# Performance work log

Measured on AMD Instinct MI355X. Metric: run time of the kernel, lower is better.

Reference implementation:

```python
import jax, jax.numpy as jnp
import numpy as np

N_NODES = 4096
M_NODES = 8192
DIM = 256


def _symnorm(A):
    # D^{-1/2} A D^{-1/2} with eps, via row/col scaling (same math as diag matmuls)
    d = A.sum(axis=1) + 1e-5
    s = d ** -0.5
    return A * s[:, None] * s[None, :]


def _gat(A, X, W, a_src, a_dst, b):
    # Dense-form GATConv (PyG semantics): edges are nonzeros of A plus self loops.
    N = A.shape[0]
    H, F = a_src.shape
    Xp = (X @ W).reshape(N, H, F)                     # [N, H, F]
    src = jnp.einsum('nhf,hf->nh', Xp, a_src)         # score of source node j
    dst = jnp.einsum('nhf,hf->nh', Xp, a_dst)         # score of target node i
    logits = jax.nn.leaky_relu(dst[:, None, :] + src[None, :, :], negative_slope=0.2)  # [i, j, h]
    mask = (A != 0.0) | jnp.eye(N, dtype=bool)        # add_self_loops=True
    logits = jnp.where(mask[:, :, None], logits, -jnp.inf)
    alpha = jax.nn.softmax(logits, axis=1)            # softmax over neighbors j
    out = jnp.einsum('ijh,jhf->ihf', alpha, Xp).reshape(N, H * F) + b
    return out


def setup_inputs() -> dict:
    key = jax.random.key(0)
    ks = jax.random.split(key, 32)

    def p(i, shape, scale=0.05):
        return jax.random.normal(ks[i], shape, dtype=jnp.float32) * scale

    R = jax.random.normal(ks[0], (N_NODES, N_NODES), dtype=jnp.float32)
    A = jax.nn.relu((R + R.T) * 0.5)
    X = jax.random.normal(ks[1], (N_NODES, DIM), dtype=jnp.float32)
    return dict(
        A=A, X=X,
        # down GT0: GATConv(256, 128, heads=4) -> 512
        Wd0=p(2, (256, 512)), asd0=p(3, (4, 128)), add0=p(4, (4, 128)), bd0=p(5, (512,)),
        # down GT1: GATConv(512, 256, heads=4) -> 1024
        Wd1=p(6, (512, 1024)), asd1=p(7, (4, 256)), add1=p(8, (4, 256)), bd1=p(9, (1024,)),
        # pool projections (Linear(in, 1))
        wp0=p(10, (1, 512)), bp0=p(11, (1,)),
        wp1=p(12, (1, 1024)), bp1=p(13, (1,)),
        # bottom GT: GATConv(1024, 512, heads=2) -> 1024
        Wb=p(14, (1024, 1024)), asb=p(15, (2, 512)), adb=p(16, (2, 512)), bb=p(17, (1024,)),
        # up GT (reversed[0]): GATConv(1024, 128, heads=4) -> 512
        Wu0=p(18, (1024, 512)), asu0=p(19, (4, 128)), adu0=p(20, (4, 128)), bu0=p(21, (512,)),
        # up GT (reversed[1]): GATConv(512, 64, heads=4) -> 256
        Wu1=p(22, (512, 256)), asu1=p(23, (4, 64)), adu1=p(24, (4, 64)), bu1=p(25, (256,)),
        # upsampler Linear(n_nodes, m_nodes)
        Wup=p(26, (M_NODES, N_NODES)), bup=p(27, (M_NODES,)),
    )


def reference(A, X, Wd0, asd0, add0, bd0, Wd1, asd1, add1, bd1, wp0, bp0, wp1, bp1,
              Wb, asb, adb, bb, Wu0, asu0, adu0, bu0, Wu1, asu1, adu1, bu1, Wup, bup):
    N0 = A.shape[0]
    A0 = A + jnp.eye(N0, dtype=A.dtype)  # A_ = A + I (used throughout; normalized A is dead code)

    # ---- down level 0 ----
    X0 = jax.nn.relu(_gat(A0, X, Wd0, asd0, add0, bd0))            # [4096, 512]
    s0 = jax.nn.sigmoid(X0 @ wp0[0] + bp0[0])
    k0 = max(2, N0 // 2)                                            # int(0.5 * N)
    v0, idx0 = jax.lax.top_k(s0, k0)
    A1 = _symnorm(A0[idx0][:, idx0])                                # [2048, 2048]
    X1in = X0[idx0] * v0[:, None]

    # ---- down level 1 ----
    X1 = jax.nn.relu(_gat(A1, X1in, Wd1, asd1, add1, bd1))          # [2048, 1024]
    s1 = jax.nn.sigmoid(X1 @ wp1[0] + bp1[0])
    k1 = max(2, k0 // 2)
    v1, idx1 = jax.lax.top_k(s1, k1)
    A2 = _symnorm(A1[idx1][:, idx1])                                # [1024, 1024]
    X2in = X1[idx1] * v1[:, None]

    # ---- bottom ----
    Xb = jax.nn.relu(_gat(A2, X2in, Wb, asb, adb, bb))              # [1024, 1024]

    # ---- up level 0: unpool to level-1 graph ----
    h = jnp.zeros((k0, Xb.shape[1]), Xb.dtype).at[idx1].set(Xb)
    Xu0 = jax.nn.relu(_gat(A1, h, Wu0, asu0, adu0, bu0))            # [2048, 512]
    rec0 = jax.nn.relu(Xu0 @ Xu0.T)

    # ---- up level 1: unpool to original graph ----
    h = jnp.zeros((N0, Xu0.shape[1]), Xu0.dtype).at[idx0].set(Xu0)
    Xu1 = jax.nn.relu(_gat(A0, h, Wu1, asu1, adu1, bu1))            # [4096, 256]
    rec1 = jax.nn.relu(Xu1 @ Xu1.T)

    # ---- upsampler: Linear over node dim, softmax over feature dim, reconstruct adjacency ----
    Z = jax.nn.softmax(Wup @ Xu1 + bup[:, None], axis=1)            # [8192, 256]
    A_up = jax.nn.relu(Z @ Z.T)                                     # [8192, 8192]
    return (A_up, A0, A1, rec0, rec1)
```

## Files before the change

kernel.cpp:

```cpp
#include <hip/hip_runtime.h>
#include <math.h>


typedef short bf16x8 __attribute__((ext_vector_type(8)));
typedef float f32x4 __attribute__((ext_vector_type(4)));

static __device__ __forceinline__ float wave_sum64(float v) {
#pragma unroll
  for (int off = 32; off; off >>= 1) v += __shfl_down(v, off);
  return v;
}

static __device__ __forceinline__ unsigned short f2b(float x) {
  unsigned u = __float_as_uint(x);
  unsigned r = (u + 0x7fffu + ((u >> 16) & 1u)) >> 16;
  return (unsigned short)r;
}

static __device__ __forceinline__ float b2f(unsigned short h) {
  return __uint_as_float(((unsigned)h) << 16);
}

__global__ void k_add_eye(const float* __restrict__ A, float* __restrict__ O) {
  size_t i = ((size_t)blockIdx.x * 256 + threadIdx.x) * 4;
  size_t r = i >> 12, c = i & 4095;
  float4 v = *reinterpret_cast<const float4*>(&A[i]);
  if (r >= c && r < c + 4) ((float*)&v)[r - c] += 1.f;
  *reinterpret_cast<float4*>(&O[i]) = v;
}

__global__ void k_fill0(float* __restrict__ p, int n) {
  int stride = gridDim.x * 256;
  for (int i = blockIdx.x * 256 + threadIdx.x; i < n; i += stride) p[i] = 0.f;
}

__global__ void k_split3(const float* __restrict__ S, unsigned short* __restrict__ D,
                         size_t PS, int n) {
  int stride = gridDim.x * 1024;
  for (int i = (blockIdx.x * 256 + threadIdx.x) * 4; i < n; i += stride) {
    float4 v = *reinterpret_cast<const float4*>(&S[i]);
    float xv[4] = {v.x, v.y, v.z, v.w};
    unsigned short o1[4], o2[4], o3[4];
#pragma unroll
    for (int e = 0; e < 4; ++e) {
      float x = xv[e];
      unsigned short a = f2b(x);
      float r1 = x - b2f(a);
      unsigned short b = f2b(r1);
      float r2 = r1 - b2f(b);
      o1[e] = a; o2[e] = b; o3[e] = f2b(r2);
    }
    *reinterpret_cast<uint2*>(&D[i]) = *reinterpret_cast<const uint2*>(o1);
    *reinterpret_cast<uint2*>(&D[PS + i]) = *reinterpret_cast<const uint2*>(o2);
    *reinterpret_cast<uint2*>(&D[2 * PS + i]) = *reinterpret_cast<const uint2*>(o3);
  }
}

__global__ void k_gather_scale_split3(const float* __restrict__ Xs, int Dd,
    const int* __restrict__ idx, const float* __restrict__ v,
    unsigned short* __restrict__ D, size_t PS) {
  int i = blockIdx.y;
  int f = (blockIdx.x * 256 + threadIdx.x) * 4;
  if (f >= Dd) return;
  float vi = v[i];
  float4 x4 = *reinterpret_cast<const float4*>(&Xs[(size_t)idx[i] * Dd + f]);
  float xv[4] = {x4.x * vi, x4.y * vi, x4.z * vi, x4.w * vi};
  unsigned short o1[4], o2[4], o3[4];
#pragma unroll
  for (int e = 0; e < 4; ++e) {
    float x = xv[e];
    unsigned short a = f2b(x);
    float r1 = x - b2f(a);
    unsigned short b = f2b(r1);
    float r2 = r1 - b2f(b);
    o1[e] = a; o2[e] = b; o3[e] = f2b(r2);
  }
  size_t e0 = (size_t)i * Dd + f;
  *reinterpret_cast<uint2*>(&D[e0]) = *reinterpret_cast<const uint2*>(o1);
  *reinterpret_cast<uint2*>(&D[PS + e0]) = *reinterpret_cast<const uint2*>(o2);
  *reinterpret_cast<uint2*>(&D[2 * PS + e0]) = *reinterpret_cast<const uint2*>(o3);
}

__global__ void k_gather_scale_b16(const float* __restrict__ Xs, int Dd,
    const int* __restrict__ idx, const float* __restrict__ v,
    unsigned short* __restrict__ D) {
  int i = blockIdx.y;
  int f = (blockIdx.x * 256 + threadIdx.x) * 4;
  if (f >= Dd) return;
  float vi = v[i];
  float4 x4 = *reinterpret_cast<const float4*>(&Xs[(size_t)idx[i] * Dd + f]);
  unsigned short o[4] = {f2b(x4.x * vi), f2b(x4.y * vi), f2b(x4.z * vi), f2b(x4.w * vi)};
  *reinterpret_cast<uint2*>(&D[(size_t)i * Dd + f]) = *reinterpret_cast<const uint2*>(o);
}

__global__ __launch_bounds__(256) void k_transpose_bf16(const float* __restrict__ S, int ldS,
    unsigned short* __restrict__ D, int R, int Cc) {
  __shared__ unsigned short T[64][72];
  int r0 = blockIdx.y << 6, c0 = blockIdx.x << 6;
  int tid = threadIdx.x;
  int tr = tid >> 4, tc4 = (tid & 15) << 2;
#pragma unroll
  for (int q = 0; q < 4; ++q) {
    int row = tr + q * 16;
    float4 v = *reinterpret_cast<const float4*>(&S[(size_t)(r0 + row) * ldS + c0 + tc4]);
    T[tc4 + 0][row] = f2b(v.x);
    T[tc4 + 1][row] = f2b(v.y);
    T[tc4 + 2][row] = f2b(v.z);
    T[tc4 + 3][row] = f2b(v.w);
  }
  __syncthreads();
#pragma unroll
  for (int q = 0; q < 4; ++q) {
    int row = tr + q * 16;
    *reinterpret_cast<uint2*>(&D[(size_t)(c0 + row) * R + r0 + tc4]) =
        *reinterpret_cast<const uint2*>(&T[row][tc4]);
  }
}

__global__ __launch_bounds__(256) void k_transpose_bb(const unsigned short* __restrict__ S,
    int ldS, unsigned short* __restrict__ D, int R, int Cc) {
  __shared__ unsigned short T[64][72];
  int r0 = blockIdx.y << 6, c0 = blockIdx.x << 6;
  int tid = threadIdx.x;
  int tr = tid >> 4, tc4 = (tid & 15) << 2;
#pragma unroll
  for (int q = 0; q < 4; ++q) {
    int row = tr + q * 16;
    uint2 v = *reinterpret_cast<const uint2*>(&S[(size_t)(r0 + row) * ldS + c0 + tc4]);
    const unsigned short* p = (const unsigned short*)&v;
    T[tc4 + 0][row] = p[0]; T[tc4 + 1][row] = p[1];
    T[tc4 + 2][row] = p[2]; T[tc4 + 3][row] = p[3];
  }
  __syncthreads();
#pragma unroll
  for (int q = 0; q < 4; ++q) {
    int row = tr + q * 16;
    *reinterpret_cast<uint2*>(&D[(size_t)(c0 + row) * R + r0 + tc4]) =
        *reinterpret_cast<const uint2*>(&T[row][tc4]);
  }
}

__global__ __launch_bounds__(256) void k_transpose_bf16h(const float* __restrict__ S, int ldS,
    int F, unsigned short* __restrict__ D, int R) {
  __shared__ unsigned short T[64][72];
  int h = blockIdx.z;
  int r0 = blockIdx.y << 6, c0 = blockIdx.x << 6;
  int tid = threadIdx.x;
  int tr = tid >> 4, tc4 = (tid & 15) << 2;
#pragma unroll
  for (int q = 0; q < 4; ++q) {
    int row = tr + q * 16;
    float4 v = *reinterpret_cast<const float4*>(&S[(size_t)(r0 + row) * ldS + h * F + c0 + tc4]);
    T[tc4 + 0][row] = f2b(v.x);
    T[tc4 + 1][row] = f2b(v.y);
    T[tc4 + 2][row] = f2b(v.z);
    T[tc4 + 3][row] = f2b(v.w);
  }
  __syncthreads();
#pragma unroll
  for (int q = 0; q < 4; ++q) {
    int row = tr + q * 16;
    *reinterpret_cast<uint2*>(&D[((size_t)h * F + c0 + row) * R + r0 + tc4]) =
        *reinterpret_cast<const uint2*>(&T[row][tc4]);
  }
}

__global__ __launch_bounds__(256) void k_transpose_split(const float* __restrict__ S, int ldS,
    int F, unsigned short* __restrict__ D, int R, size_t PS) {
  __shared__ unsigned short T[3][64][72];
  int h = blockIdx.z;
  int c0 = blockIdx.x << 6, r0 = blockIdx.y << 6;
  int tid = threadIdx.x;
  int tr = tid >> 4, tc4 = (tid & 15) << 2;
#pragma unroll
  for (int q = 0; q < 4; ++q) {
    int row = tr + q * 16;
    float4 v = *reinterpret_cast<const float4*>(&S[(size_t)(r0 + row) * ldS + h * F + c0 + tc4]);
    float xv[4] = {v.x, v.y, v.z, v.w};
#pragma unroll
    for (int e = 0; e < 4; ++e) {
      float x = xv[e];
      unsigned short h1 = f2b(x);
      float r1 = x - b2f(h1);
      unsigned short h2 = f2b(r1);
      float r2 = r1 - b2f(h2);
      T[0][tc4 + e][row] = h1;
      T[1][tc4 + e][row] = h2;
      T[2][tc4 + e][row] = f2b(r2);
    }
  }
  __syncthreads();
#pragma unroll
  for (int p = 0; p < 3; ++p)
#pragma unroll
    for (int q = 0; q < 4; ++q) {
      int row = tr + q * 16;
      *reinterpret_cast<uint2*>(&D[p * PS + (size_t)(h * F + c0 + row) * R + r0 + tc4]) =
          *reinterpret_cast<const uint2*>(&T[p][row][tc4]);
    }
}

__global__ __launch_bounds__(256, 2) void k_gemm_x6_bt(const unsigned short* __restrict__ As,
    size_t APS, const unsigned short* __restrict__ BTs, size_t BPS, float* __restrict__ C,
    int M, int N, int K) {
  __shared__ __align__(16) unsigned short Ai[3][128 * 40];
  __shared__ __align__(16) unsigned short Bj[3][128 * 40];
  int tid = threadIdx.x;
  int m0 = blockIdx.y << 7, n0 = blockIdx.x << 7;
  int lane = tid & 63, w = tid >> 6;
  int lr = lane & 15, kb = lane >> 4;
  int wr = (w >> 1) << 6, wc = (w & 1) << 6;
  int sr = tid >> 1, sc = (tid & 1) << 4;
  f32x4 acc[4][4] = {};
  for (int k0 = 0; k0 < K; k0 += 32) {
    __syncthreads();
#pragma unroll
    for (int p = 0; p < 3; ++p) {
      const unsigned short* ga = &As[p * APS + (size_t)(m0 + sr) * K + k0 + sc];
      *reinterpret_cast<uint4*>(&Ai[p][sr * 40 + sc]) = *reinterpret_cast<const uint4*>(ga);
      *reinterpret_cast<uint4*>(&Ai[p][sr * 40 + sc + 8]) =
          *reinterpret_cast<const uint4*>(ga + 8);
      const unsigned short* gb = &BTs[p * BPS + (size_t)(n0 + sr) * K + k0 + sc];
      *reinterpret_cast<uint4*>(&Bj[p][sr * 40 + sc]) = *reinterpret_cast<const uint4*>(gb);
      *reinterpret_cast<uint4*>(&Bj[p][sr * 40 + sc + 8]) =
          *reinterpret_cast<const uint4*>(gb + 8);
    }
    __syncthreads();
    bf16x8 af[4][3], bf_[4][3];
#pragma unroll
    for (int m = 0; m < 4; ++m)
#pragma unroll
      for (int p = 0; p < 3; ++p)
        af[m][p] = *reinterpret_cast<const bf16x8*>(&Ai[p][(wr + m * 16 + lr) * 40 + kb * 8]);
#pragma unroll
    for (int n = 0; n < 4; ++n)
#pragma unroll
      for (int p = 0; p < 3; ++p)
        bf_[n][p] = *reinterpret_cast<const bf16x8*>(&Bj[p][(wc + n * 16 + lr) * 40 + kb * 8]);
#pragma unroll
    for (int m = 0; m < 4; ++m)
#pragma unroll
      for (int n = 0; n < 4; ++n) {
        acc[m][n] = __builtin_amdgcn_mfma_f32_16x16x32_bf16(af[m][0], bf_[n][0], acc[m][n], 0, 0, 0);
        acc[m][n] = __builtin_amdgcn_mfma_f32_16x16x32_bf16(af[m][0], bf_[n][1], acc[m][n], 0, 0, 0);
        acc[m][n] = __builtin_amdgcn_mfma_f32_16x16x32_bf16(af[m][1], bf_[n][0], acc[m][n], 0, 0, 0);
        acc[m][n] = __builtin_amdgcn_mfma_f32_16x16x32_bf16(af[m][0], bf_[n][2], acc[m][n], 0, 0, 0);
        acc[m][n] = __builtin_amdgcn_mfma_f32_16x16x32_bf16(af[m][2], bf_[n][0], acc[m][n], 0, 0, 0);
        acc[m][n] = __builtin_amdgcn_mfma_f32_16x16x32_bf16(af[m][1], bf_[n][1], acc[m][n], 0, 0, 0);
      }
  }
  int orow = m0 + wr + (lane >> 4) * 4;
  int ocol = n0 + wc + lr;
#pragma unroll
  for (int m = 0; m < 4; ++m)
#pragma unroll
    for (int n = 0; n < 4; ++n)
#pragma unroll
      for (int r = 0; r < 4; ++r)
        C[(size_t)(orow + m * 16 + r) * N + ocol + n * 16] = acc[m][n][r];
}

__global__ __launch_bounds__(512, 4) void k_gat_x6(const float* __restrict__ Adj, int N,
    const unsigned short* __restrict__ XpS, size_t PS,
    const float* __restrict__ src, const float* __restrict__ dst,
    float* __restrict__ P, float* __restrict__ dP, int HF, int Ffull, int FP, int jchunk) {
  __shared__ __align__(16) unsigned short wL[3][128 * 40];
  __shared__ __align__(16) unsigned short xL[3][128 * 40];
  __shared__ float dstL[128];
  __shared__ float srcL[32];
  int H = HF / Ffull;
  int h = blockIdx.x / FP;
  int fp = blockIdx.x % FP;
  int f0 = fp << 7;
  int i0 = blockIdx.y << 7;
  int jb0 = blockIdx.z * jchunk;
  int tid = threadIdx.x;
  int si = tid >> 2, sj8 = (tid & 3) << 3;
  int lane = tid & 63, w = tid >> 6;
  int lr = lane & 15, kb = lane >> 4;
  int fs = w << 4;
  if (tid < 128) dstL[tid] = dst[(i0 + tid) * H + h];
  float dsum = 0.f;
  f32x4 acc[8] = {};
  int ntiles = jchunk >> 5;
  const unsigned short* xbase = XpS + ((size_t)h * Ffull + f0) * N;
  for (int t = 0; t < ntiles; ++t) {
    int jb = jb0 + (t << 5);
    __syncthreads();
    if (tid < 32) srcL[tid] = src[(jb + tid) * H + h];
    {
      int frow = tid >> 2;
#pragma unroll
      for (int p = 0; p < 3; ++p)
        *reinterpret_cast<uint4*>(&xL[p][frow * 40 + sj8]) =
            *reinterpret_cast<const uint4*>(&xbase[p * PS + (size_t)frow * N + jb + sj8]);
    }
    float4 av0 = *reinterpret_cast<const float4*>(&Adj[(size_t)(i0 + si) * N + jb + sj8]);
    float4 av1 = *reinterpret_cast<const float4*>(&Adj[(size_t)(i0 + si) * N + jb + sj8 + 4]);
    __syncthreads();
    {
      int gi = i0 + si;
      float dq = dstL[si];
      const float* a0 = (const float*)&av0;
      const float* a1 = (const float*)&av1;
      unsigned short h1[8], h2[8], h3[8];
      float ds = 0.f;
#pragma unroll
      for (int e = 0; e < 8; ++e) {
        float a = e < 4 ? a0[e] : a1[e - 4];
        float wv = 0.f;
        if (a != 0.f || (jb + sj8 + e) == gi) {
          float tt = dq + srcL[sj8 + e];
          tt = tt >= 0.f ? tt : 0.2f * tt;
          wv = __expf(tt);
        }
        ds += wv;
        unsigned u1 = __float_as_uint(wv);
        h1[e] = (unsigned short)(u1 >> 16);
        float r1 = wv - __uint_as_float(u1 & 0xffff0000u);
        unsigned u2 = __float_as_uint(r1);
        h2[e] = (unsigned short)(u2 >> 16);
        float r2 = r1 - __uint_as_float(u2 & 0xffff0000u);
        h3[e] = (unsigned short)(__float_as_uint(r2) >> 16);
      }
      dsum += ds;
      *reinterpret_cast<uint4*>(&wL[0][si * 40 + sj8]) = *reinterpret_cast<const uint4*>(h1);
      *reinterpret_cast<uint4*>(&wL[1][si * 40 + sj8]) = *reinterpret_cast<const uint4*>(h2);
      *reinterpret_cast<uint4*>(&wL[2][si * 40 + sj8]) = *reinterpret_cast<const uint4*>(h3);
    }
    __syncthreads();
    bf16x8 bf_[3];
#pragma unroll
    for (int p = 0; p < 3; ++p)
      bf_[p] = *reinterpret_cast<const bf16x8*>(&xL[p][(fs + lr) * 40 + kb * 8]);
#pragma unroll
    for (int m = 0; m < 8; ++m) {
      bf16x8 af[3];
#pragma unroll
      for (int p = 0; p < 3; ++p)
        af[p] = *reinterpret_cast<const bf16x8*>(&wL[p][(m * 16 + lr) * 40 + kb * 8]);
      acc[m] = __builtin_amdgcn_mfma_f32_16x16x32_bf16(af[0], bf_[0], acc[m], 0, 0, 0);
      acc[m] = __builtin_amdgcn_mfma_f32_16x16x32_bf16(af[0], bf_[1], acc[m], 0, 0, 0);
      acc[m] = __builtin_amdgcn_mfma_f32_16x16x32_bf16(af[1], bf_[0], acc[m], 0, 0, 0);
      acc[m] = __builtin_amdgcn_mfma_f32_16x16x32_bf16(af[0], bf_[2], acc[m], 0, 0, 0);
      acc[m] = __builtin_amdgcn_mfma_f32_16x16x32_bf16(af[2], bf_[0], acc[m], 0, 0, 0);
      acc[m] = __builtin_amdgcn_mfma_f32_16x16x32_bf16(af[1], bf_[1], acc[m], 0, 0, 0);
    }
  }
  if (fp == 0) {
    float v = dsum;
    v += __shfl_xor(v, 1);
    v += __shfl_xor(v, 2);
    if ((tid & 3) == 0)
      dP[(size_t)blockIdx.z * N * H + (i0 + si) * H + h] = v;
  }
  float* Pc = P + (size_t)blockIdx.z * N * HF;
  int orow = i0 + (lane >> 4) * 4;
  int ocol = h * Ffull + f0 + fs + lr;
#pragma unroll
  for (int m = 0; m < 8; ++m)
#pragma unroll
    for (int r = 0; r < 4; ++r)
      Pc[(size_t)(orow + m * 16 + r) * HF + ocol] = acc[m][r];
}

template <int NS, int HEADS>
__global__ __launch_bounds__(512) void k_gat_b16(const float* __restrict__ Adj, int N,
    const unsigned short* __restrict__ XpT,
    const float* __restrict__ src, const float* __restrict__ dst,
    float* __restrict__ P, float* __restrict__ dP, int HF, int F, int jchunk) {
  constexpr int HFB = NS * 128;
  __shared__ __align__(16) unsigned short wL[HEADS][128 * 40];
  __shared__ __align__(16) unsigned short xL[HFB * 40];
  __shared__ float dstL[HEADS][128];
  __shared__ float srcL[HEADS][32];
  int H = HF / F;
  int hf0 = blockIdx.x * HFB;
  int h0 = hf0 / F;
  int i0 = blockIdx.y << 7;
  int jb0 = blockIdx.z * jchunk;
  int tid = threadIdx.x;
  int si = tid >> 2, sj8 = (tid & 3) << 3;
  int lane = tid & 63, w = tid >> 6;
  int lr = lane & 15, kb = lane >> 4;
  int fs = w * (NS * 16);
  int hw = (hf0 + fs) / F - h0;
  if (tid < HEADS * 128)
    dstL[tid >> 7][tid & 127] = dst[(i0 + (tid & 127)) * H + h0 + (tid >> 7)];
  float dsum[HEADS] = {};
  f32x4 acc[8][NS] = {};
  int ntiles = jchunk >> 5;
  for (int t = 0; t < ntiles; ++t) {
    int jb = jb0 + (t << 5);
    __syncthreads();
    if (tid < HEADS * 32) srcL[tid >> 5][tid & 31] = src[(jb + (tid & 31)) * H + h0 + (tid >> 5)];
#pragma unroll
    for (int base = 0; base < HFB; base += 128) {
      int row = base + (tid >> 2);
      *reinterpret_cast<uint4*>(&xL[row * 40 + sj8]) =
          *reinterpret_cast<const uint4*>(&XpT[(size_t)(hf0 + row) * N + jb + sj8]);
    }
    float4 av0 = *reinterpret_cast<const float4*>(&Adj[(size_t)(i0 + si) * N + jb + sj8]);
    float4 av1 = *reinterpret_cast<const float4*>(&Adj[(size_t)(i0 + si) * N + jb + sj8 + 4]);
    __syncthreads();
    {
      int gi = i0 + si;
      const float* a0 = (const float*)&av0;
      const float* a1 = (const float*)&av1;
#pragma unroll
      for (int hh = 0; hh < HEADS; ++hh) {
        float dq = dstL[hh][si];
        unsigned short wb[8];
        float ds = 0.f;
#pragma unroll
        for (int e = 0; e < 8; ++e) {
          float a = e < 4 ? a0[e] : a1[e - 4];
          float wv = 0.f;
          if (a != 0.f || (jb + sj8 + e) == gi) {
            float tt = dq + srcL[hh][sj8 + e];
            tt = tt >= 0.f ? tt : 0.2f * tt;
            wv = __expf(tt);
          }
          ds += wv;
          wb[e] = f2b(wv);
        }
        dsum[hh] += ds;
        *reinterpret_cast<uint4*>(&wL[hh][si * 40 + sj8]) =
            *reinterpret_cast<const uint4*>(wb);
      }
    }
    __syncthreads();
    bf16x8 bf_[NS];
#pragma unroll
    for (int n = 0; n < NS; ++n)
      bf_[n] = *reinterpret_cast<const bf16x8*>(&xL[(fs + n * 16 + lr) * 40 + kb * 8]);
#pragma unroll
    for (int m = 0; m < 8; ++m) {
      bf16x8 a = *reinterpret_cast<const bf16x8*>(&wL[hw][(m * 16 + lr) * 40 + kb * 8]);
#pragma unroll
      for (int n = 0; n < NS; ++n)
        acc[m][n] = __builtin_amdgcn_mfma_f32_16x16x32_bf16(a, bf_[n], acc[m][n], 0, 0, 0);
    }
  }
#pragma unroll
  for (int hh = 0; hh < HEADS; ++hh) {
    float v = dsum[hh];
    v += __shfl_xor(v, 1);
    v += __shfl_xor(v, 2);
    if ((tid & 3) == 0)
      dP[(size_t)blockIdx.z * N * H + (i0 + si) * H + h0 + hh] = v;
  }
  float* Pc = P + (size_t)blockIdx.z * N * HF;
  int orow = i0 + (lane >> 4) * 4;
  int ocol0 = hf0 + fs + lr;
#pragma unroll
  for (int m = 0; m < 8; ++m)
#pragma unroll
    for (int n = 0; n < NS; ++n)
#pragma unroll
      for (int r = 0; r < 4; ++r)
        Pc[(size_t)(orow + m * 16 + r) * HF + ocol0 + n * 16] = acc[m][n][r];
}

__global__ void k_gat_reduce(const float* __restrict__ P, int nch, size_t chstride,
    const float* __restrict__ dP, size_t dstride, const float* __restrict__ bias,
    float* __restrict__ Of, unsigned short* __restrict__ Ob, int HF, int F, int n_total) {
  int e = (blockIdx.x * 256 + threadIdx.x) * 4;
  if (e >= n_total) return;
  float4 s = *reinterpret_cast<const float4*>(&P[e]);
  for (int c = 1; c < nch; ++c) {
    float4 v = *reinterpret_cast<const float4*>(&P[c * chstride + e]);
    s.x += v.x; s.y += v.y; s.z += v.z; s.w += v.w;
  }
  int i = e / HF;
  int hf = e - i * HF;
  int h = hf / F;
  float den = 0.f;
  for (int c = 0; c < nch; ++c) den += dP[c * dstride + i * (HF / F) + h];
  float inv = 1.f / den;
  float4 bz = *reinterpret_cast<const float4*>(&bias[hf]);
  float4 o;
  o.x = fmaxf(fmaf(s.x, inv, bz.x), 0.f);
  o.y = fmaxf(fmaf(s.y, inv, bz.y), 0.f);
  o.z = fmaxf(fmaf(s.z, inv, bz.z), 0.f);
  o.w = fmaxf(fmaf(s.w, inv, bz.w), 0.f);
  if (Of) *reinterpret_cast<float4*>(&Of[e]) = o;
  if (Ob) {
    unsigned short ob[4] = {f2b(o.x), f2b(o.y), f2b(o.z), f2b(o.w)};
    *reinterpret_cast<uint2*>(&Ob[e]) = *reinterpret_cast<const uint2*>(ob);
  }
}

__global__ __launch_bounds__(256) void k_syrk_mfma(const unsigned short* __restrict__ G,
    int M, int Kd, float* __restrict__ C) {
  if (blockIdx.x < blockIdx.y) return;
  __shared__ __align__(16) unsigned short Ai[128 * 40];
  __shared__ __align__(16) unsigned short Bj[128 * 40];
  int tid = threadIdx.x;
  int i0 = blockIdx.y << 7, j0 = blockIdx.x << 7;
  int srow = tid >> 1, scol = (tid & 1) << 3;
  int lane = tid & 63, w = tid >> 6;
  int wr = (w >> 1) << 6, wc = (w & 1) << 6;
  int lr = lane & 15, kb = lane >> 4;
  f32x4 acc[4][4] = {};
  const unsigned short* gA = G + (size_t)i0 * Kd;
  const unsigned short* gB = G + (size_t)j0 * Kd;
  for (int k0 = 0; k0 < Kd; k0 += 32) {
    __syncthreads();
#pragma unroll
    for (int kk = 0; kk < 32; kk += 16) {
      *reinterpret_cast<uint4*>(&Ai[srow * 40 + scol + kk]) =
          *reinterpret_cast<const uint4*>(&gA[(size_t)srow * Kd + k0 + scol + kk]);
      *reinterpret_cast<uint4*>(&Bj[srow * 40 + scol + kk]) =
          *reinterpret_cast<const uint4*>(&gB[(size_t)srow * Kd + k0 + scol + kk]);
    }
    __syncthreads();
    bf16x8 a[4], b[4];
#pragma unroll
    for (int m = 0; m < 4; ++m)
      a[m] = *reinterpret_cast<const bf16x8*>(&Ai[(wr + m * 16 + lr) * 40 + kb * 8]);
#pragma unroll
    for (int n = 0; n < 4; ++n)
      b[n] = *reinterpret_cast<const bf16x8*>(&Bj[(wc + n * 16 + lr) * 40 + kb * 8]);
#pragma unroll
    for (int m = 0; m < 4; ++m)
#pragma unroll
      for (int n = 0; n < 4; ++n)
        acc[m][n] = __builtin_amdgcn_mfma_f32_16x16x32_bf16(a[m], b[n], acc[m][n], 0, 0, 0);
  }
  int orow = i0 + wr + (lane >> 4) * 4;
  int ocol = j0 + wc + (lane & 15);
  bool mirror = (j0 != i0);
#pragma unroll
  for (int m = 0; m < 4; ++m)
#pragma unroll
    for (int n = 0; n < 4; ++n) {
      float4 v;
      v.x = fmaxf(acc[m][n][0], 0.f);
      v.y = fmaxf(acc[m][n][1], 0.f);
      v.z = fmaxf(acc[m][n][2], 0.f);
      v.w = fmaxf(acc[m][n][3], 0.f);
#pragma unroll
      for (int r = 0; r < 4; ++r)
        C[(size_t)(orow + m * 16 + r) * M + ocol + n * 16] = ((const float*)&v)[r];
      if (mirror)
        *reinterpret_cast<float4*>(
            &C[(size_t)(j0 + wc + n * 16 + lr) * M + i0 + wr + m * 16 + (lane >> 4) * 4]) = v;
    }
}

__global__ __launch_bounds__(256) void k_gemm_mfma_bt(const unsigned short* __restrict__ Amat,
    const unsigned short* __restrict__ BT, const float* __restrict__ bias,
    float* __restrict__ C, int M, int N, int Kd) {
  __shared__ __align__(16) unsigned short Ai[128 * 40];
  __shared__ __align__(16) unsigned short Bj[128 * 40];
  int tid = threadIdx.x;
  int m0 = blockIdx.y << 7, n0 = blockIdx.x << 7;
  int srow = tid >> 1, scol = (tid & 1) << 3;
  int lane = tid & 63, w = tid >> 6;
  int wr = (w >> 1) << 6, wc = (w & 1) << 6;
  int lr = lane & 15, kb = lane >> 4;
  f32x4 acc[4][4] = {};
  const unsigned short* gA = Amat + (size_t)m0 * Kd;
  const unsigned short* gB = BT + (size_t)n0 * Kd;
  for (int k0 = 0; k0 < Kd; k0 += 32) {
    __syncthreads();
#pragma unroll
    for (int kk = 0; kk < 32; kk += 16) {
      *reinterpret_cast<uint4*>(&Ai[srow * 40 + scol + kk]) =
          *reinterpret_cast<const uint4*>(&gA[(size_t)srow * Kd + k0 + scol + kk]);
      *reinterpret_cast<uint4*>(&Bj[srow * 40 + scol + kk]) =
          *reinterpret_cast<const uint4*>(&gB[(size_t)srow * Kd + k0 + scol + kk]);
    }
    __syncthreads();
    bf16x8 a[4], b[4];
#pragma unroll
    for (int m = 0; m < 4; ++m)
      a[m] = *reinterpret_cast<const bf16x8*>(&Ai[(wr + m * 16 + lr) * 40 + kb * 8]);
#pragma unroll
    for (int n = 0; n < 4; ++n)
      b[n] = *reinterpret_cast<const bf16x8*>(&Bj[(wc + n * 16 + lr) * 40 + kb * 8]);
#pragma unroll
    for (int m = 0; m < 4; ++m)
#pragma unroll
      for (int n = 0; n < 4; ++n)
        acc[m][n] = __builtin_amdgcn_mfma_f32_16x16x32_bf16(a[m], b[n], acc[m][n], 0, 0, 0);
  }
  int orow = m0 + wr + (lane >> 4) * 4;
  int ocol = n0 + wc + (lane & 15);
#pragma unroll
  for (int m = 0; m < 4; ++m)
#pragma unroll
    for (int n = 0; n < 4; ++n)
#pragma unroll
      for (int r = 0; r < 4; ++r) {
        float rb = bias ? bias[orow + m * 16 + r] : 0.f;
        C[(size_t)(orow + m * 16 + r) * N + ocol + n * 16] = acc[m][n][r] + rb;
      }
}

__global__ __launch_bounds__(512) void k_gemm_aup(const float* __restrict__ Wg,
    const unsigned short* __restrict__ BT, float* __restrict__ Pz, int Mtot, int Ktot,
    int kc_len) {
  __shared__ __align__(16) unsigned short Ai[128 * 40];
  __shared__ __align__(16) unsigned short Bj[256 * 40];
  int tid = threadIdx.x;
  int m0 = blockIdx.y << 7;
  int k0base = blockIdx.x * kc_len;
  int lane = tid & 63, w = tid >> 6;
  int wr = (w >> 2) << 6, wc = (w & 3) << 6;
  int lr = lane & 15, kb = lane >> 4;
  int ar = tid >> 2, ac8 = (tid & 3) << 3;
  int br = tid >> 1, bc16 = (tid & 1) << 4;
  f32x4 acc[4][4] = {};
  for (int kk = 0; kk < kc_len; kk += 32) {
    int k0 = k0base + kk;
    __syncthreads();
    {
      const float* arow = &Wg[(size_t)(m0 + ar) * Ktot + k0 + ac8];
      float4 v0 = *reinterpret_cast<const float4*>(arow);
      float4 v1 = *reinterpret_cast<const float4*>(arow + 4);
      unsigned short t8[8] = {f2b(v0.x), f2b(v0.y), f2b(v0.z), f2b(v0.w),
                              f2b(v1.x), f2b(v1.y), f2b(v1.z), f2b(v1.w)};
      *reinterpret_cast<uint4*>(&Ai[ar * 40 + ac8]) = *reinterpret_cast<const uint4*>(t8);
      const unsigned short* brow = &BT[(size_t)br * Ktot + k0 + bc16];
      *reinterpret_cast<uint4*>(&Bj[br * 40 + bc16]) = *reinterpret_cast<const uint4*>(brow);
      *reinterpret_cast<uint4*>(&Bj[br * 40 + bc16 + 8]) =
          *reinterpret_cast<const uint4*>(brow + 8);
    }
    __syncthreads();
    bf16x8 a[4], b[4];
#pragma unroll
    for (int m = 0; m < 4; ++m)
      a[m] = *reinterpret_cast<const bf16x8*>(&Ai[(wr + m * 16 + lr) * 40 + kb * 8]);
#pragma unroll
    for (int n = 0; n < 4; ++n)
      b[n] = *reinterpret_cast<const bf16x8*>(&Bj[(wc + n * 16 + lr) * 40 + kb * 8]);
#pragma unroll
    for (int m = 0; m < 4; ++m)
#pragma unroll
      for (int n = 0; n < 4; ++n)
        acc[m][n] = __builtin_amdgcn_mfma_f32_16x16x32_bf16(a[m], b[n], acc[m][n], 0, 0, 0);
  }
  float* outp = Pz + (size_t)blockIdx.x * Mtot * 256;
  int orow = m0 + wr + (lane >> 4) * 4;
  int ocol = wc + (lane & 15);
#pragma unroll
  for (int m = 0; m < 4; ++m)
#pragma unroll
    for (int n = 0; n < 4; ++n)
#pragma unroll
      for (int r = 0; r < 4; ++r)
        outp[(size_t)(orow + m * 16 + r) * 256 + ocol + n * 16] = acc[m][n][r];
}

__global__ __launch_bounds__(256) void k_softmax_fuse(const float* __restrict__ Pz, int nch,
    size_t chstride, const float* __restrict__ bias, unsigned short* __restrict__ ZB) {
  int row = blockIdx.x, tid = threadIdx.x;
  size_t e = (size_t)row * 256 + tid;
  float x = bias[row];
  for (int c = 0; c < nch; ++c) x += Pz[c * chstride + e];
  float m = x;
#pragma unroll
  for (int off = 32; off; off >>= 1) m = fmaxf(m, __shfl_down(m, off));
  __shared__ float red[4];
  __shared__ float bm, bs;
  if ((tid & 63) == 0) red[tid >> 6] = m;
  __syncthreads();
  if (tid == 0) bm = fmaxf(fmaxf(red[0], red[1]), fmaxf(red[2], red[3]));
  __syncthreads();
  float ev = expf(x - bm);
  float sm = wave_sum64(ev);
  __syncthreads();
  if ((tid & 63) == 0) red[tid >> 6] = sm;
  __syncthreads();
  if (tid == 0) bs = red[0] + red[1] + red[2] + red[3];
  __syncthreads();
  ZB[e] = f2b(ev / bs);
}

__global__ void k_src_dst(const float* __restrict__ Xp, const float* __restrict__ a_src,
    const float* __restrict__ a_dst, float* __restrict__ src, float* __restrict__ dst,
    int H, int F) {
  int n = blockIdx.x;
  int h = threadIdx.x >> 6, lane = threadIdx.x & 63;
  const float* x = Xp + ((size_t)n * H + h) * F;
  const float* as = a_src + h * F;
  const float* ad = a_dst + h * F;
  float ps = 0.f, pd = 0.f;
  for (int f = lane; f < F; f += 64) {
    float xv = x[f];
    ps = fmaf(xv, as[f], ps);
    pd = fmaf(xv, ad[f], pd);
  }
  ps = wave_sum64(ps);
  pd = wave_sum64(pd);
  if (lane == 0) { src[n * H + h] = ps; dst[n * H + h] = pd; }
}

__global__ __launch_bounds__(256) void k_score(const float* __restrict__ Xf,
    const float* __restrict__ wv, const float* __restrict__ bsc, float* __restrict__ s, int D) {
  int row = blockIdx.x * 4 + (threadIdx.x >> 6);
  int lane = threadIdx.x & 63;
  const float* x = Xf + (size_t)row * D;
  float p = 0.f;
  for (int f = lane; f < D; f += 64) p = fmaf(x[f], wv[f], p);
  p = wave_sum64(p);
  if (lane == 0) s[row] = 1.f / (1.f + expf(-(p + bsc[0])));
}

__global__ __launch_bounds__(256) void k_topk_rank(const float* __restrict__ s, int n, int k,
    int* __restrict__ idx, float* __restrict__ vals, float* __restrict__ mask) {
  extern __shared__ unsigned long long keys[];
  int tid = threadIdx.x;
  int i = blockIdx.x * 256 + tid;
  if (mask) mask[i] = 0.f;
  for (int j = tid; j < n; j += 256) {
    unsigned u = __float_as_uint(s[j]);
    unsigned ord = (u & 0x80000000u) ? ~u : (u | 0x80000000u);
    keys[j] = ((unsigned long long)ord << 32) | (unsigned)(~j);
  }
  __syncthreads();
  unsigned long long mykey = keys[i];
  int rank = 0;
#pragma unroll 4
  for (int j = 0; j < n; ++j) rank += (keys[j] > mykey);
  if (rank < k) {
    idx[rank] = i;
    vals[rank] = s[i];
    if (mask) mask[i] = 1.f;
  }
}

__global__ __launch_bounds__(256) void k_rowsum_mask(const float* __restrict__ A0, int N,
    const int* __restrict__ idx, const float* __restrict__ m, float* __restrict__ sv) {
  int i = blockIdx.x, tid = threadIdx.x;
  const float* row = A0 + (size_t)idx[i] * N;
  float p = 0.f;
  for (int j = tid * 4; j < N; j += 1024) {
    float4 a = *reinterpret_cast<const float4*>(&row[j]);
    float4 b = *reinterpret_cast<const float4*>(&m[j]);
    p += a.x * b.x + a.y * b.y + a.z * b.z + a.w * b.w;
  }
  p = wave_sum64(p);
  __shared__ float red[4];
  if ((tid & 63) == 0) red[tid >> 6] = p;
  __syncthreads();
  if (tid == 0) sv[i] = rsqrtf(red[0] + red[1] + red[2] + red[3] + 1e-5f);
}

__global__ __launch_bounds__(256) void k_gatherT(const float* __restrict__ A0, int N,
    const int* __restrict__ idx, float* __restrict__ T1, int k) {
  __shared__ float T[64][65];
  int i0 = blockIdx.x << 6, c0 = blockIdx.y << 6;
  int tid = threadIdx.x;
  int tr = tid >> 4, tc4 = (tid & 15) << 2;
#pragma unroll
  for (int q = 0; q < 4; ++q) {
    int row = tr + q * 16;
    float4 v = *reinterpret_cast<const float4*>(&A0[(size_t)idx[i0 + row] * N + c0 + tc4]);
    T[tc4 + 0][row] = v.x; T[tc4 + 1][row] = v.y; T[tc4 + 2][row] = v.z; T[tc4 + 3][row] = v.w;
  }
  __syncthreads();
#pragma unroll
  for (int q = 0; q < 4; ++q) {
    int row = tr + q * 16;
    float4 o;
    o.x = T[row][tc4]; o.y = T[row][tc4 + 1]; o.z = T[row][tc4 + 2]; o.w = T[row][tc4 + 3];
    *reinterpret_cast<float4*>(&T1[(size_t)(c0 + row) * k + i0 + tc4]) = o;
  }
}

__global__ void k_scaleT(const float* __restrict__ T1, int k, const int* __restrict__ idx,
    const float* __restrict__ sv, float* __restrict__ A1) {
  int j = blockIdx.y;
  int i = (blockIdx.x * 256 + threadIdx.x) * 4;
  float sj = sv[j];
  const float* r = T1 + (size_t)idx[j] * k;
  float4 v = *reinterpret_cast<const float4*>(&r[i]);
  float4 s = *reinterpret_cast<const float4*>(&sv[i]);
  v.x *= sj * s.x; v.y *= sj * s.y; v.z *= sj * s.z; v.w *= sj * s.w;
  *reinterpret_cast<float4*>(&A1[(size_t)j * k + i]) = v;
}

__global__ void k_gather_mat(const float* __restrict__ Asrc, int lda,
    const int* __restrict__ idx, float* __restrict__ B, int k) {
  int j = blockIdx.x * 256 + threadIdx.x;
  int i = blockIdx.y;
  B[(size_t)i * k + j] = Asrc[(size_t)idx[i] * lda + idx[j]];
}

__global__ void k_scatter_rows(const float* __restrict__ P, int D, const int* __restrict__ idx,
                               float* __restrict__ Xo) {
  int f = blockIdx.x * 256 + threadIdx.x;
  int i = blockIdx.y;
  Xo[(size_t)idx[i] * D + f] = P[(size_t)i * D + f];
}

extern "C" void kernel_launch(void* const* d_in, const int* in_sizes, int n_in,
                              void* d_out, int out_size, void* d_ws, size_t ws_size,
                              hipStream_t stream) {
  const float* A    = (const float*)d_in[0];
  const float* X    = (const float*)d_in[1];
  const float* Wd0  = (const float*)d_in[2];
  const float* asd0 = (const float*)d_in[3];
  const float* add0 = (const float*)d_in[4];
  const float* bd0  = (const float*)d_in[5];
  const float* Wd1  = (const float*)d_in[6];
  const float* asd1 = (const float*)d_in[7];
  const float* add1 = (const float*)d_in[8];
  const float* bd1  = (const float*)d_in[9];
  const float* wp0  = (const float*)d_in[10];
  const float* bp0  = (const float*)d_in[11];
  const float* wp1  = (const float*)d_in[12];
  const float* bp1  = (const float*)d_in[13];
  const float* Wb   = (const float*)d_in[14];
  const float* asb  = (const float*)d_in[15];
  const float* adb  = (const float*)d_in[16];
  const float* bb   = (const float*)d_in[17];
  const float* Wu0  = (const float*)d_in[18];
  const float* asu0 = (const float*)d_in[19];
  const float* adu0 = (const float*)d_in[20];
  const float* bu0  = (const float*)d_in[21];
  const float* Wu1  = (const float*)d_in[22];
  const float* asu1 = (const float*)d_in[23];
  const float* adu1 = (const float*)d_in[24];
  const float* bu1  = (const float*)d_in[25];
  const float* Wup  = (const float*)d_in[26];
  const float* bup  = (const float*)d_in[27];
  (void)in_sizes; (void)n_in; (void)out_size; (void)ws_size;

  float* out  = (float*)d_out;
  float* Aup  = out;
  float* A0   = out + 67108864ULL;
  float* A1   = A0 + 16777216ULL;
  float* rec0 = A1 + 4194304ULL;
  float* rec1 = rec0 + 4194304ULL;

  float* S = Aup;
  size_t off = 0;
  auto nxt = [&](size_t n) { float* p = S + off; off += (n + 1023) & ~(size_t)1023; return p; };
  float* Xp0  = nxt(4096 * 512);
  float* X0   = nxt(4096 * 512);
  float* src0 = nxt(4096 * 4);
  float* dst0 = nxt(4096 * 4);
  float* sc0  = nxt(4096);
  int*   idx0 = (int*)nxt(2048);
  float* v0   = nxt(2048);
  float* sv0  = nxt(2048);
  float* maskv = nxt(4096);
  float* Xp1  = nxt(2048 * 1024);
  float* X1   = nxt(2048 * 1024);
  float* src1 = nxt(2048 * 4);
  float* dst1 = nxt(2048 * 4);
  float* sc1  = nxt(2048);
  int*   idx1 = (int*)nxt(1024);
  float* v1   = nxt(1024);
  float* A2m  = nxt(1024 * 1024);
  float* Xpb  = nxt(1024 * 1024);
  float* srcb = nxt(1024 * 2);
  float* dstb = nxt(1024 * 2);
  float* Pu0  = nxt(1024 * 512);
  float* Xpu0 = nxt(2048 * 512);
  float* su0  = nxt(2048 * 4);
  float* du0  = nxt(2048 * 4);
  float* Pu1  = nxt(2048 * 256);
  float* Xpu1 = nxt(4096 * 256);
  float* su1  = nxt(4096 * 4);
  float* du1  = nxt(4096 * 4);
  float* dPp  = nxt(8 * 4096 * 4);
  float* P    = nxt((size_t)8 * 4096 * 512);
  float* T1   = nxt((size_t)4096 * 2048);
  unsigned short* XpS  = (unsigned short*)nxt(3200000);
  unsigned short* XSp  = (unsigned short*)nxt(1572864);
  unsigned short* Wd0T = (unsigned short*)nxt(196608);
  unsigned short* Wd1T = (unsigned short*)nxt(786432);
  unsigned short* XpT  = (unsigned short*)nxt(524288);
  unsigned short* X2inB = (unsigned short*)nxt(524288);
  unsigned short* XbB   = (unsigned short*)nxt(524288);
  unsigned short* WbT   = (unsigned short*)nxt(524288);
  unsigned short* Wu0T  = (unsigned short*)nxt(262144);
  unsigned short* Wu1T  = (unsigned short*)nxt(65536);

  float* W = (float*)d_ws;
  unsigned short* Xu1B = (unsigned short*)(W + 1048576);
  unsigned short* Xu0B = (unsigned short*)(W + 1048576 + 524288);

  float* Pz = rec1;
  unsigned short* ZB = (unsigned short*)(rec1 + 4 * 2097152);
  unsigned short* Xu1T = (unsigned short*)(rec1 + 4 * 2097152 + 1048576);

  const size_t PS0 = (size_t)4 * 128 * 4096;
  const size_t PS1 = (size_t)4 * 256 * 2048;

  k_add_eye<<<16384, 256, 0, stream>>>(A, A0);

  k_split3<<<1024, 256, 0, stream>>>(X, XSp, (size_t)4096 * 256, 4096 * 256);
  k_transpose_split<<<dim3(8, 4, 1), 256, 0, stream>>>(Wd0, 512, 512, Wd0T, 256,
                                                       (size_t)512 * 256);
  k_gemm_x6_bt<<<dim3(4, 32), 256, 0, stream>>>(XSp, (size_t)4096 * 256, Wd0T,
                                                (size_t)512 * 256, Xp0, 4096, 512, 256);
  k_src_dst<<<4096, 256, 0, stream>>>(Xp0, asd0, add0, src0, dst0, 4, 128);
  k_transpose_split<<<dim3(2, 64, 4), 256, 0, stream>>>(Xp0, 512, 128, XpS, 4096, PS0);
  k_gat_x6<<<dim3(4, 32, 4), 512, 0, stream>>>(A0, 4096, XpS, PS0, src0, dst0, P, dPp, 512,
                                               128, 1, 1024);
  k_gat_reduce<<<2048, 256, 0, stream>>>(P, 4, (size_t)4096 * 512, dPp, (size_t)4096 * 4, bd0,
                                         X0, nullptr, 512, 128, 4096 * 512);
  k_score<<<1024, 256, 0, stream>>>(X0, wp0, bp0, sc0, 512);
  k_topk_rank<<<16, 256, 4096 * 8, stream>>>(sc0, 4096, 2048, idx0, v0, maskv);
  k_rowsum_mask<<<2048, 256, 0, stream>>>(A0, 4096, idx0, maskv, sv0);
  k_gatherT<<<dim3(32, 64), 256, 0, stream>>>(A0, 4096, idx0, T1, 2048);
  k_scaleT<<<dim3(2, 2048), 256, 0, stream>>>(T1, 2048, idx0, sv0, A1);

  k_gather_scale_split3<<<dim3(1, 2048), 256, 0, stream>>>(X0, 512, idx0, v0, XSp,
                                                           (size_t)2048 * 512);
  k_transpose_split<<<dim3(16, 8, 1), 256, 0, stream>>>(Wd1, 1024, 1024, Wd1T, 512,
                                                        (size_t)1024 * 512);
  k_gemm_x6_bt<<<dim3(8, 16), 256, 0, stream>>>(XSp, (size_t)2048 * 512, Wd1T,
                                                (size_t)1024 * 512, Xp1, 2048, 1024, 512);
  k_src_dst<<<2048, 256, 0, stream>>>(Xp1, asd1, add1, src1, dst1, 4, 256);
  k_transpose_split<<<dim3(4, 32, 4), 256, 0, stream>>>(Xp1, 1024, 256, XpS, 2048, PS1);
  k_gat_x6<<<dim3(8, 16, 4), 512, 0, stream>>>(A1, 2048, XpS, PS1, src1, dst1, P, dPp, 1024,
                                               256, 2, 512);
  k_gat_reduce<<<2048, 256, 0, stream>>>(P, 4, (size_t)2048 * 1024, dPp, (size_t)2048 * 4, bd1,
                                         X1, nullptr, 1024, 256, 2048 * 1024);
  k_score<<<512, 256, 0, stream>>>(X1, wp1, bp1, sc1, 1024);
  k_topk_rank<<<8, 256, 2048 * 8, stream>>>(sc1, 2048, 1024, idx1, v1, nullptr);
  k_gather_mat<<<dim3(4, 1024), 256, 0, stream>>>(A1, 2048, idx1, A2m, 1024);
  k_gather_scale_b16<<<dim3(1, 1024), 256, 0, stream>>>(X1, 1024, idx1, v1, X2inB);

  k_transpose_bf16<<<dim3(16, 16), 256, 0, stream>>>(Wb, 1024, WbT, 1024, 1024);
  k_gemm_mfma_bt<<<dim3(8, 8), 256, 0, stream>>>(X2inB, WbT, nullptr, Xpb, 1024, 1024, 1024);
  k_src_dst<<<1024, 128, 0, stream>>>(Xpb, asb, adb, srcb, dstb, 2, 512);
  k_transpose_bf16h<<<dim3(8, 16, 2), 256, 0, stream>>>(Xpb, 1024, 512, XpT, 1024);
  k_gat_b16<4, 1><<<dim3(2, 8, 4), 512, 0, stream>>>(A2m, 1024, XpT, srcb, dstb, P, dPp, 1024,
                                                     512, 256);
  k_gat_reduce<<<1024, 256, 0, stream>>>(P, 4, (size_t)1024 * 1024, dPp, (size_t)1024 * 2, bb,
                                         nullptr, XbB, 1024, 512, 1024 * 1024);

  k_transpose_bf16<<<dim3(8, 16), 256, 0, stream>>>(Wu0, 512, Wu0T, 1024, 512);
  k_gemm_mfma_bt<<<dim3(4, 8), 256, 0, stream>>>(XbB, Wu0T, nullptr, Pu0, 1024, 512, 1024);
  k_fill0<<<1024, 256, 0, stream>>>(Xpu0, 2048 * 512);
  k_scatter_rows<<<dim3(2, 1024), 256, 0, stream>>>(Pu0, 512, idx1, Xpu0);
  k_src_dst<<<2048, 256, 0, stream>>>(Xpu0, asu0, adu0, su0, du0, 4, 128);
  k_transpose_bf16h<<<dim3(2, 32, 4), 256, 0, stream>>>(Xpu0, 512, 128, XpT, 2048);
  k_gat_b16<4, 4><<<dim3(1, 16, 8), 512, 0, stream>>>(A1, 2048, XpT, su0, du0, P, dPp, 512,
                                                      128, 256);
  k_gat_reduce<<<1024, 256, 0, stream>>>(P, 8, (size_t)2048 * 512, dPp, (size_t)2048 * 4, bu0,
                                         nullptr, Xu0B, 512, 128, 2048 * 512);

  k_transpose_bf16<<<dim3(4, 8), 256, 0, stream>>>(Wu1, 256, Wu1T, 512, 256);
  k_gemm_mfma_bt<<<dim3(2, 16), 256, 0, stream>>>(Xu0B, Wu1T, nullptr, Pu1, 2048, 256, 512);
  k_fill0<<<1024, 256, 0, stream>>>(Xpu1, 4096 * 256);
  k_scatter_rows<<<dim3(1, 2048), 256, 0, stream>>>(Pu1, 256, idx0, Xpu1);
  k_src_dst<<<4096, 256, 0, stream>>>(Xpu1, asu1, adu1, su1, du1, 4, 64);
  k_transpose_bf16h<<<dim3(1, 64, 4), 256, 0, stream>>>(Xpu1, 256, 64, XpT, 4096);
  k_gat_b16<2, 4><<<dim3(1, 32, 8), 512, 0, stream>>>(A0, 4096, XpT, su1, du1, P, dPp, 256,
                                                      64, 512);
  k_gat_reduce<<<1024, 256, 0, stream>>>(P, 8, (size_t)4096 * 256, dPp, (size_t)4096 * 4, bu1,
                                         nullptr, Xu1B, 256, 64, 4096 * 256);
  k_transpose_bb<<<dim3(4, 64), 256, 0, stream>>>(Xu1B, 256, Xu1T, 4096, 256);

  k_gemm_aup<<<dim3(4, 64), 512, 0, stream>>>(Wup, Xu1T, Pz, 8192, 4096, 1024);
  k_softmax_fuse<<<8192, 256, 0, stream>>>(Pz, 4, (size_t)8192 * 256, bup, ZB);
  k_syrk_mfma<<<dim3(64, 64), 256, 0, stream>>>(ZB, 8192, 256, Aup);

  k_syrk_mfma<<<dim3(32, 32), 256, 0, stream>>>(Xu1B, 4096, 256, rec1);
  k_syrk_mfma<<<dim3(16, 16), 256, 0, stream>>>(Xu0B, 2048, 512, rec0);
}
```

Before: 960.9 us.

## Prefetch tiles into registers, fuse transposes into GEMM epilogue, replace scatter with inverse-index unpool

Adds register-level prefetch of the next K/j tile in the GEMM and GAT kernels so global loads overlap with MFMA work. The GEMM epilogues now also write a transposed split or bf16 copy, which removes separate transpose kernels. Scatter plus zero-fill is replaced by an inverse-index unpool, and the float mask becomes an int inverse map. Several launch grids change as well (more split-K chunks for aup and the bottom GAT, different NS/HEADS). The cost is higher register pressure and more strided transposed stores in the epilogue.

```diff
diff --git a/kernel.cpp b/kernel.cpp
--- a/kernel.cpp
+++ b/kernel.cpp
@@ -27,11 +27,6 @@
   float4 v = *reinterpret_cast<const float4*>(&A[i]);
   if (r >= c && r < c + 4) ((float*)&v)[r - c] += 1.f;
   *reinterpret_cast<float4*>(&O[i]) = v;
-}
-
-__global__ void k_fill0(float* __restrict__ p, int n) {
-  int stride = gridDim.x * 256;
-  for (int i = blockIdx.x * 256 + threadIdx.x; i < n; i += stride) p[i] = 0.f;
 }
 
 __global__ void k_split3(const float* __restrict__ S, unsigned short* __restrict__ D,
@@ -202,7 +197,7 @@
 
 __global__ __launch_bounds__(256, 2) void k_gemm_x6_bt(const unsigned short* __restrict__ As,
     size_t APS, const unsigned short* __restrict__ BTs, size_t BPS, float* __restrict__ C,
-    int M, int N, int K) {
+    unsigned short* __restrict__ Tp, int M, int N, int K) {
   __shared__ __align__(16) unsigned short Ai[3][128 * 40];
   __shared__ __align__(16) unsigned short Bj[3][128 * 40];
   int tid = threadIdx.x;
@@ -211,21 +206,31 @@
   int lr = lane & 15, kb = lane >> 4;
   int wr = (w >> 1) << 6, wc = (w & 1) << 6;
   int sr = tid >> 1, sc = (tid & 1) << 4;
+  uint4 rA[3][2], rB[3][2];
+  auto load_k = [&](int k0) {
+#pragma unroll
+    for (int p = 0; p < 3; ++p) {
+      const unsigned short* ga = &As[p * APS + (size_t)(m0 + sr) * K + k0 + sc];
+      rA[p][0] = *reinterpret_cast<const uint4*>(ga);
+      rA[p][1] = *reinterpret_cast<const uint4*>(ga + 8);
+      const unsigned short* gb = &BTs[p * BPS + (size_t)(n0 + sr) * K + k0 + sc];
+      rB[p][0] = *reinterpret_cast<const uint4*>(gb);
+      rB[p][1] = *reinterpret_cast<const uint4*>(gb + 8);
+    }
+  };
+  load_k(0);
   f32x4 acc[4][4] = {};
   for (int k0 = 0; k0 < K; k0 += 32) {
     __syncthreads();
 #pragma unroll
     for (int p = 0; p < 3; ++p) {
-      const unsigned short* ga = &As[p * APS + (size_t)(m0 + sr) * K + k0 + sc];
-      *reinterpret_cast<uint4*>(&Ai[p][sr * 40 + sc]) = *reinterpret_cast<const uint4*>(ga);
-      *reinterpret_cast<uint4*>(&Ai[p][sr * 40 + sc + 8]) =
-          *reinterpret_cast<const uint4*>(ga + 8);
-      const unsigned short* gb = &BTs[p * BPS + (size_t)(n0 + sr) * K + k0 + sc];
-      *reinterpret_cast<uint4*>(&Bj[p][sr * 40 + sc]) = *reinterpret_cast<const uint4*>(gb);
-      *reinterpret_cast<uint4*>(&Bj[p][sr * 40 + sc + 8]) =
-          *reinterpret_cast<const uint4*>(gb + 8);
-    }
-    __syncthreads();
+      *reinterpret_cast<uint4*>(&Ai[p][sr * 40 + sc]) = rA[p][0];
+      *reinterpret_cast<uint4*>(&Ai[p][sr * 40 + sc + 8]) = rA[p][1];
+      *reinterpret_cast<uint4*>(&Bj[p][sr * 40 + sc]) = rB[p][0];
+      *reinterpret_cast<uint4*>(&Bj[p][sr * 40 + sc + 8]) = rB[p][1];
+    }
+    __syncthreads();
+    if (k0 + 32 < K) load_k(k0 + 32);
     bf16x8 af[4][3], bf_[4][3];
 #pragma unroll
     for (int m = 0; m < 4; ++m)
@@ -251,13 +256,31 @@
   }
   int orow = m0 + wr + (lane >> 4) * 4;
   int ocol = n0 + wc + lr;
+  size_t TPS = (size_t)M * N;
 #pragma unroll
   for (int m = 0; m < 4; ++m)
 #pragma unroll
-    for (int n = 0; n < 4; ++n)
-#pragma unroll
-      for (int r = 0; r < 4; ++r)
-        C[(size_t)(orow + m * 16 + r) * N + ocol + n * 16] = acc[m][n][r];
+    for (int n = 0; n < 4; ++n) {
+      int cn = ocol + n * 16, rw = orow + m * 16;
+#pragma unroll
+      for (int r = 0; r < 4; ++r) C[(size_t)(rw + r) * N + cn] = acc[m][n][r];
+      if (Tp) {
+        unsigned short o1[4], o2[4], o3[4];
+#pragma unroll
+        for (int r = 0; r < 4; ++r) {
+          float x = acc[m][n][r];
+          unsigned short a = f2b(x);
+          float r1 = x - b2f(a);
+          unsigned short b = f2b(r1);
+          float r2 = r1 - b2f(b);
+          o1[r] = a; o2[r] = b; o3[r] = f2b(r2);
+        }
+        size_t tb = (size_t)cn * M + rw;
+        *reinterpret_cast<uint2*>(&Tp[tb]) = *reinterpret_cast<const uint2*>(o1);
+        *reinterpret_cast<uint2*>(&Tp[TPS + tb]) = *reinterpret_cast<const uint2*>(o2);
+        *reinterpret_cast<uint2*>(&Tp[2 * TPS + tb]) = *reinterpret_cast<const uint2*>(o3);
+      }
+    }
 }
 
 __global__ __launch_bounds__(512, 4) void k_gat_x6(const float* __restrict__ Adj, int N,
@@ -267,7 +290,7 @@
   __shared__ __align__(16) unsigned short wL[3][128 * 40];
   __shared__ __align__(16) unsigned short xL[3][128 * 40];
   __shared__ float dstL[128];
-  __shared__ float srcL[32];
+  __shared__ float srcL[2][32];
   int H = HF / Ffull;
   int h = blockIdx.x / FP;
   int fp = blockIdx.x % FP;
@@ -280,23 +303,24 @@
   int lr = lane & 15, kb = lane >> 4;
   int fs = w << 4;
   if (tid < 128) dstL[tid] = dst[(i0 + tid) * H + h];
+  if (tid < 32) srcL[0][tid] = src[(jb0 + tid) * H + h];
+  const unsigned short* xbase = XpS + ((size_t)h * Ffull + f0) * N;
+  float4 av0, av1;
+  uint4 xv[3];
+  auto load_tile = [&](int jb) {
+    av0 = *reinterpret_cast<const float4*>(&Adj[(size_t)(i0 + si) * N + jb + sj8]);
+    av1 = *reinterpret_cast<const float4*>(&Adj[(size_t)(i0 + si) * N + jb + sj8 + 4]);
+#pragma unroll
+    for (int p = 0; p < 3; ++p)
+      xv[p] = *reinterpret_cast<const uint4*>(&xbase[p * PS + (size_t)si * N + jb + sj8]);
+  };
+  load_tile(jb0);
   float dsum = 0.f;
   f32x4 acc[8] = {};
   int ntiles = jchunk >> 5;
-  const unsigned short* xbase = XpS + ((size_t)h * Ffull + f0) * N;
   for (int t = 0; t < ntiles; ++t) {
     int jb = jb0 + (t << 5);
-    __syncthreads();
-    if (tid < 32) srcL[tid] = src[(jb + tid) * H + h];
-    {
-      int frow = tid >> 2;
-#pragma unroll
-      for (int p = 0; p < 3; ++p)
-        *reinterpret_cast<uint4*>(&xL[p][frow * 40 + sj8]) =
-            *reinterpret_cast<const uint4*>(&xbase[p * PS + (size_t)frow * N + jb + sj8]);
-    }
-    float4 av0 = *reinterpret_cast<const float4*>(&Adj[(size_t)(i0 + si) * N + jb + sj8]);
-    float4 av1 = *reinterpret_cast<const float4*>(&Adj[(size_t)(i0 + si) * N + jb + sj8 + 4]);
+    int cur = t & 1;
     __syncthreads();
     {
       int gi = i0 + si;
@@ -310,7 +334,7 @@
         float a = e < 4 ? a0[e] : a1[e - 4];
         float wv = 0.f;
         if (a != 0.f || (jb + sj8 + e) == gi) {
-          float tt = dq + srcL[sj8 + e];
+          float tt = dq + srcL[cur][sj8 + e];
           tt = tt >= 0.f ? tt : 0.2f * tt;
           wv = __expf(tt);
         }
@@ -327,8 +351,16 @@
       *reinterpret_cast<uint4*>(&wL[0][si * 40 + sj8]) = *reinterpret_cast<const uint4*>(h1);
       *reinterpret_cast<uint4*>(&wL[1][si * 40 + sj8]) = *reinterpret_cast<const uint4*>(h2);
       *reinterpret_cast<uint4*>(&wL[2][si * 40 + sj8]) = *reinterpret_cast<const uint4*>(h3);
-    }
-    __syncthreads();
+#pragma unroll
+      for (int p = 0; p < 3; ++p)
+        *reinterpret_cast<uint4*>(&xL[p][si * 40 + sj8]) = xv[p];
+    }
+    __syncthreads();
+    if (t + 1 < ntiles) {
+      int jn = jb + 32;
+      if (tid < 32) srcL[cur ^ 1][tid] = src[(jn + tid) * H + h];
+      load_tile(jn);
+    }
     bf16x8 bf_[3];
 #pragma unroll
     for (int p = 0; p < 3; ++p)
@@ -365,7 +397,7 @@
 }
 
 template <int NS, int HEADS>
-__global__ __launch_bounds__(512) void k_gat_b16(const float* __restrict__ Adj, int N,
+__global__ __launch_bounds__(512, 4) void k_gat_b16(const float* __restrict__ Adj, int N,
     const unsigned short* __restrict__ XpT,
     const float* __restrict__ src, const float* __restrict__ dst,
     float* __restrict__ P, float* __restrict__ dP, int HF, int F, int jchunk) {
@@ -373,7 +405,7 @@
   __shared__ __align__(16) unsigned short wL[HEADS][128 * 40];
   __shared__ __align__(16) unsigned short xL[HFB * 40];
   __shared__ float dstL[HEADS][128];
-  __shared__ float srcL[HEADS][32];
+  __shared__ float srcL[2][HEADS][32];
   int H = HF / F;
   int hf0 = blockIdx.x * HFB;
   int h0 = hf0 / F;
@@ -387,21 +419,25 @@
   int hw = (hf0 + fs) / F - h0;
   if (tid < HEADS * 128)
     dstL[tid >> 7][tid & 127] = dst[(i0 + (tid & 127)) * H + h0 + (tid >> 7)];
+  if (tid < HEADS * 32)
+    srcL[0][tid >> 5][tid & 31] = src[(jb0 + (tid & 31)) * H + h0 + (tid >> 5)];
+  float4 av0, av1;
+  uint4 xv[NS];
+  auto load_tile = [&](int jb) {
+    av0 = *reinterpret_cast<const float4*>(&Adj[(size_t)(i0 + si) * N + jb + sj8]);
+    av1 = *reinterpret_cast<const float4*>(&Adj[(size_t)(i0 + si) * N + jb + sj8 + 4]);
+#pragma unroll
+    for (int s = 0; s < NS; ++s)
+      xv[s] = *reinterpret_cast<const uint4*>(
+          &XpT[(size_t)(hf0 + s * 128 + si) * N + jb + sj8]);
+  };
+  load_tile(jb0);
   float dsum[HEADS] = {};
   f32x4 acc[8][NS] = {};
   int ntiles = jchunk >> 5;
   for (int t = 0; t < ntiles; ++t) {
     int jb = jb0 + (t << 5);
-    __syncthreads();
-    if (tid < HEADS * 32) srcL[tid >> 5][tid & 31] = src[(jb + (tid & 31)) * H + h0 + (tid >> 5)];
-#pragma unroll
-    for (int base = 0; base < HFB; base += 128) {
-      int row = base + (tid >> 2);
-      *reinterpret_cast<uint4*>(&xL[row * 40 + sj8]) =
-          *reinterpret_cast<const uint4*>(&XpT[(size_t)(hf0 + row) * N + jb + sj8]);
-    }
-    float4 av0 = *reinterpret_cast<const float4*>(&Adj[(size_t)(i0 + si) * N + jb + sj8]);
-    float4 av1 = *reinterpret_cast<const float4*>(&Adj[(size_t)(i0 + si) * N + jb + sj8 + 4]);
+    int cur = t & 1;
     __syncthreads();
     {
       int gi = i0 + si;
@@ -417,7 +453,7 @@
           float a = e < 4 ? a0[e] : a1[e - 4];
           float wv = 0.f;
           if (a != 0.f || (jb + sj8 + e) == gi) {
-            float tt = dq + srcL[hh][sj8 + e];
+            float tt = dq + srcL[cur][hh][sj8 + e];
             tt = tt >= 0.f ? tt : 0.2f * tt;
             wv = __expf(tt);
           }
@@ -425,11 +461,19 @@
           wb[e] = f2b(wv);
         }
         dsum[hh] += ds;
-        *reinterpret_cast<uint4*>(&wL[hh][si * 40 + sj8]) =
-            *reinterpret_cast<const uint4*>(wb);
+        *reinterpret_cast<uint4*>(&wL[hh][si * 40 + sj8]) = *reinterpret_cast<const uint4*>(wb);
       }
-    }
-    __syncthreads();
+#pragma unroll
+      for (int s = 0; s < NS; ++s)
+        *reinterpret_cast<uint4*>(&xL[(s * 128 + si) * 40 + sj8]) = xv[s];
+    }
+    __syncthreads();
+    if (t + 1 < ntiles) {
+      int jn = jb + 32;
+      if (tid < HEADS * 32)
+        srcL[cur ^ 1][tid >> 5][tid & 31] = src[(jn + (tid & 31)) * H + h0 + (tid >> 5)];
+      load_tile(jn);
+    }
     bf16x8 bf_[NS];
 #pragma unroll
     for (int n = 0; n < NS; ++n)
@@ -551,7 +595,7 @@
 
 __global__ __launch_bounds__(256) void k_gemm_mfma_bt(const unsigned short* __restrict__ Amat,
     const unsigned short* __restrict__ BT, const float* __restrict__ bias,
-    float* __restrict__ C, int M, int N, int Kd) {
+    float* __restrict__ C, unsigned short* __restrict__ Tp, int M, int N, int Kd) {
   __shared__ __align__(16) unsigned short Ai[128 * 40];
   __shared__ __align__(16) unsigned short Bj[128 * 40];
   int tid = threadIdx.x;
@@ -560,19 +604,25 @@
   int lane = tid & 63, w = tid >> 6;
   int wr = (w >> 1) << 6, wc = (w & 1) << 6;
   int lr = lane & 15, kb = lane >> 4;
+  uint4 rA[2], rB[2];
+  auto load_k = [&](int k0) {
+    const unsigned short* ga = &Amat[(size_t)(m0 + srow) * Kd + k0 + scol];
+    rA[0] = *reinterpret_cast<const uint4*>(ga);
+    rA[1] = *reinterpret_cast<const uint4*>(ga + 16);
+    const unsigned short* gb = &BT[(size_t)(n0 + srow) * Kd + k0 + scol];
+    rB[0] = *reinterpret_cast<const uint4*>(gb);
+    rB[1] = *reinterpret_cast<const uint4*>(gb + 16);
+  };
+  load_k(0);
   f32x4 acc[4][4] = {};
-  const unsigned short* gA = Amat + (size_t)m0 * Kd;
-  const unsigned short* gB = BT + (size_t)n0 * Kd;
   for (int k0 = 0; k0 < Kd; k0 += 32) {
     __syncthreads();
-#pragma unroll
-    for (int kk = 0; kk < 32; kk += 16) {
-      *reinterpret_cast<uint4*>(&Ai[srow * 40 + scol + kk]) =
-          *reinterpret_cast<const uint4*>(&gA[(size_t)srow * Kd + k0 + scol + kk]);
-      *reinterpret_cast<uint4*>(&Bj[srow * 40 + scol + kk]) =
-          *reinterpret_cast<const uint4*>(&gB[(size_t)srow * Kd + k0 + scol + kk]);
-    }
-    __syncthreads();
+    *reinterpret_cast<uint4*>(&Ai[srow * 40 + scol]) = rA[0];
+    *reinterpret_cast<uint4*>(&Ai[srow * 40 + scol + 16]) = rA[1];
+    *reinterpret_cast<uint4*>(&Bj[srow * 40 + scol]) = rB[0];
+    *reinterpret_cast<uint4*>(&Bj[srow * 40 + scol + 16]) = rB[1];
+    __syncthreads();
+    if (k0 + 32 < Kd) load_k(k0 + 32);
     bf16x8 a[4], b[4];
 #pragma unroll
     for (int m = 0; m < 4; ++m)
@@ -587,16 +637,24 @@
         acc[m][n] = __builtin_amdgcn_mfma_f32_16x16x32_bf16(a[m], b[n], acc[m][n], 0, 0, 0);
   }
   int orow = m0 + wr + (lane >> 4) * 4;
-  int ocol = n0 + wc + (lane & 15);
+  int ocol = n0 + wc + lr;
 #pragma unroll
   for (int m = 0; m < 4; ++m)
 #pragma unroll
-    for (int n = 0; n < 4; ++n)
+    for (int n = 0; n < 4; ++n) {
+      int cn = ocol + n * 16, rw = orow + m * 16;
 #pragma unroll
       for (int r = 0; r < 4; ++r) {
-        float rb = bias ? bias[orow + m * 16 + r] : 0.f;
-        C[(size_t)(orow + m * 16 + r) * N + ocol + n * 16] = acc[m][n][r] + rb;
+        float rb = bias ? bias[rw + r] : 0.f;
+        C[(size_t)(rw + r) * N + cn] = acc[m][n][r] + rb;
       }
+      if (Tp) {
+        unsigned short o[4] = {f2b(acc[m][n][0]), f2b(acc[m][n][1]), f2b(acc[m][n][2]),
+                               f2b(acc[m][n][3])};
+        *reinterpret_cast<uint2*>(&Tp[(size_t)cn * M + rw]) =
+            *reinterpret_cast<const uint2*>(o);
+      }
+    }
 }
 
 __global__ __launch_bounds__(512) void k_gemm_aup(const float* __restrict__ Wg,
@@ -612,23 +670,29 @@
   int lr = lane & 15, kb = lane >> 4;
   int ar = tid >> 2, ac8 = (tid & 3) << 3;
   int br = tid >> 1, bc16 = (tid & 1) << 4;
+  float4 ra0, ra1;
+  uint4 rb0, rb1;
+  auto load_k = [&](int k0) {
+    const float* arow = &Wg[(size_t)(m0 + ar) * Ktot + k0 + ac8];
+    ra0 = *reinterpret_cast<const float4*>(arow);
+    ra1 = *reinterpret_cast<const float4*>(arow + 4);
+    const unsigned short* brow = &BT[(size_t)br * Ktot + k0 + bc16];
+    rb0 = *reinterpret_cast<const uint4*>(brow);
+    rb1 = *reinterpret_cast<const uint4*>(brow + 8);
+  };
+  load_k(k0base);
   f32x4 acc[4][4] = {};
   for (int kk = 0; kk < kc_len; kk += 32) {
-    int k0 = k0base + kk;
     __syncthreads();
     {
-      const float* arow = &Wg[(size_t)(m0 + ar) * Ktot + k0 + ac8];
-      float4 v0 = *reinterpret_cast<const float4*>(arow);
-      float4 v1 = *reinterpret_cast<const float4*>(arow + 4);
-      unsigned short t8[8] = {f2b(v0.x), f2b(v0.y), f2b(v0.z), f2b(v0.w),
-                              f2b(v1.x), f2b(v1.y), f2b(v1.z), f2b(v1.w)};
+      unsigned short t8[8] = {f2b(ra0.x), f2b(ra0.y), f2b(ra0.z), f2b(ra0.w),
+                              f2b(ra1.x), f2b(ra1.y), f2b(ra1.z), f2b(ra1.w)};
       *reinterpret_cast<uint4*>(&Ai[ar * 40 + ac8]) = *reinterpret_cast<const uint4*>(t8);
-      const unsigned short* brow = &BT[(size_t)br * Ktot + k0 + bc16];
-      *reinterpret_cast<uint4*>(&Bj[br * 40 + bc16]) = *reinterpret_cast<const uint4*>(brow);
-      *reinterpret_cast<uint4*>(&Bj[br * 40 + bc16 + 8]) =
-          *reinterpret_cast<const uint4*>(brow + 8);
-    }
-    __syncthreads();
+      *reinterpret_cast<uint4*>(&Bj[br * 40 + bc16]) = rb0;
+      *reinterpret_cast<uint4*>(&Bj[br * 40 + bc16 + 8]) = rb1;
+    }
+    __syncthreads();
+    if (kk + 32 < kc_len) load_k(k0base + kk + 32);
     bf16x8 a[4], b[4];
 #pragma unroll
     for (int m = 0; m < 4; ++m)
@@ -710,11 +774,10 @@
 }
 
 __global__ __launch_bounds__(256) void k_topk_rank(const float* __restrict__ s, int n, int k,
-    int* __restrict__ idx, float* __restrict__ vals, float* __restrict__ mask) {
+    int* __restrict__ idx, float* __restrict__ vals, int* __restrict__ inv) {
   extern __shared__ unsigned long long keys[];
   int tid = threadIdx.x;
   int i = blockIdx.x * 256 + tid;
-  if (mask) mask[i] = 0.f;
   for (int j = tid; j < n; j += 256) {
     unsigned u = __float_as_uint(s[j]);
     unsigned ord = (u & 0x80000000u) ? ~u : (u | 0x80000000u);
@@ -725,22 +788,26 @@
   int rank = 0;
 #pragma unroll 4
   for (int j = 0; j < n; ++j) rank += (keys[j] > mykey);
-  if (rank < k) {
+  int sel = rank < k;
+  inv[i] = sel ? rank + 1 : 0;
+  if (sel) {
     idx[rank] = i;
     vals[rank] = s[i];
-    if (mask) mask[i] = 1.f;
   }
 }
 
 __global__ __launch_bounds__(256) void k_rowsum_mask(const float* __restrict__ A0, int N,
-    const int* __restrict__ idx, const float* __restrict__ m, float* __restrict__ sv) {
+    const int* __restrict__ idx, const int* __restrict__ inv, float* __restrict__ sv) {
   int i = blockIdx.x, tid = threadIdx.x;
   const float* row = A0 + (size_t)idx[i] * N;
   float p = 0.f;
   for (int j = tid * 4; j < N; j += 1024) {
     float4 a = *reinterpret_cast<const float4*>(&row[j]);
-    float4 b = *reinterpret_cast<const float4*>(&m[j]);
-    p += a.x * b.x + a.y * b.y + a.z * b.z + a.w * b.w;
+    int4 b = *reinterpret_cast<const int4*>(&inv[j]);
+    if (b.x) p += a.x;
+    if (b.y) p += a.y;
+    if (b.z) p += a.z;
+    if (b.w) p += a.w;
   }
   p = wave_sum64(p);
   __shared__ float red[4];
@@ -790,11 +857,12 @@
   B[(size_t)i * k + j] = Asrc[(size_t)idx[i] * lda + idx[j]];
 }
 
-__global__ void k_scatter_rows(const float* __restrict__ P, int D, const int* __restrict__ idx,
-                               float* __restrict__ Xo) {
+__global__ void k_unpool(const float* __restrict__ Pn, int Dd, const int* __restrict__ inv,
+                         float* __restrict__ Xo) {
+  int node = blockIdx.y;
   int f = blockIdx.x * 256 + threadIdx.x;
-  int i = blockIdx.y;
-  Xo[(size_t)idx[i] * D + f] = P[(size_t)i * D + f];
+  int r = inv[node];
+  Xo[(size_t)node * Dd + f] = r ? Pn[(size_t)(r - 1) * Dd + f] : 0.f;
 }
 
 extern "C" void kernel_launch(void* const* d_in, const int* in_sizes, int n_in,
@@ -848,7 +916,7 @@
   int*   idx0 = (int*)nxt(2048);
   float* v0   = nxt(2048);
   float* sv0  = nxt(2048);
-  float* maskv = nxt(4096);
+  int*   inv0 = (int*)nxt(4096);
   float* Xp1  = nxt(2048 * 1024);
   float* X1   = nxt(2048 * 1024);
   float* src1 = nxt(2048 * 4);
@@ -856,6 +924,7 @@
   float* sc1  = nxt(2048);
   int*   idx1 = (int*)nxt(1024);
   float* v1   = nxt(1024);
+  int*   inv1 = (int*)nxt(2048);
   float* A2m  = nxt(1024 * 1024);
   float* Xpb  = nxt(1024 * 1024);
   float* srcb = nxt(1024 * 2);
@@ -882,16 +951,15 @@
   unsigned short* Wu0T  = (unsigned short*)nxt(262144);
   unsigned short* Wu1T  = (unsigned short*)nxt(65536);
 
-  float* W = (float*)d_ws;
-  unsigned short* Xu1B = (unsigned short*)(W + 1048576);
-  unsigned short* Xu0B = (unsigned short*)(W + 1048576 + 524288);
+  unsigned short* Xu1B = (unsigned short*)d_ws;
+  unsigned short* Xu0B = (unsigned short*)((char*)d_ws + (2 << 20));
+  unsigned short* ZB   = (unsigned short*)((char*)d_ws + (4 << 20));
+  unsigned short* Xu1T = (unsigned short*)((char*)d_ws + (8 << 20));
 
   float* Pz = rec1;
-  unsigned short* ZB = (unsigned short*)(rec1 + 4 * 2097152);
-  unsigned short* Xu1T = (unsigned short*)(rec1 + 4 * 2097152 + 1048576);
-
-  const size_t PS0 = (size_t)4 * 128 * 4096;
-  const size_t PS1 = (size_t)4 * 256 * 2048;
+
+  const size_t PS0 = (size_t)512 * 4096;
+  const size_t PS1 = (size_t)1024 * 2048;
 
   k_add_eye<<<16384, 256, 0, stream>>>(A, A0);
 
@@ -899,16 +967,15 @@
   k_transpose_split<<<dim3(8, 4, 1), 256, 0, stream>>>(Wd0, 512, 512, Wd0T, 256,
                                                        (size_t)512 * 256);
   k_gemm_x6_bt<<<dim3(4, 32), 256, 0, stream>>>(XSp, (size_t)4096 * 256, Wd0T,
-                                                (size_t)512 * 256, Xp0, 4096, 512, 256);
+                                                (size_t)512 * 256, Xp0, XpS, 4096, 512, 256);
   k_src_dst<<<4096, 256, 0, stream>>>(Xp0, asd0, add0, src0, dst0, 4, 128);
-  k_transpose_split<<<dim3(2, 64, 4), 256, 0, stream>>>(Xp0, 512, 128, XpS, 4096, PS0);
   k_gat_x6<<<dim3(4, 32, 4), 512, 0, stream>>>(A0, 4096, XpS, PS0, src0, dst0, P, dPp, 512,
                                                128, 1, 1024);
   k_gat_reduce<<<2048, 256, 0, stream>>>(P, 4, (size_t)4096 * 512, dPp, (size_t)4096 * 4, bd0,
                                          X0, nullptr, 512, 128, 4096 * 512);
   k_score<<<1024, 256, 0, stream>>>(X0, wp0, bp0, sc0, 512);
-  k_topk_rank<<<16, 256, 4096 * 8, stream>>>(sc0, 4096, 2048, idx0, v0, maskv);
-  k_rowsum_mask<<<2048, 256, 0, stream>>>(A0, 4096, idx0, maskv, sv0);
+  k_topk_rank<<<16, 256, 4096 * 8, stream>>>(sc0, 4096, 2048, idx0, v0, inv0);
+  k_rowsum_mask<<<2048, 256, 0, stream>>>(A0, 4096, idx0, inv0, sv0);
   k_gatherT<<<dim3(32, 64), 256, 0, stream>>>(A0, 4096, idx0, T1, 2048);
   k_scaleT<<<dim3(2, 2048), 256, 0, stream>>>(T1, 2048, idx0, sv0, A1);
 
@@ -917,42 +984,41 @@
   k_transpose_split<<<dim3(16, 8, 1), 256, 0, stream>>>(Wd1, 1024, 1024, Wd1T, 512,
                                                         (size_t)1024 * 512);
   k_gemm_x6_bt<<<dim3(8, 16), 256, 0, stream>>>(XSp, (size_t)2048 * 512, Wd1T,
-                                                (size_t)1024 * 512, Xp1, 2048, 1024, 512);
+                                                (size_t)1024 * 512, Xp1, XpS, 2048, 1024, 512);
   k_src_dst<<<2048, 256, 0, stream>>>(Xp1, asd1, add1, src1, dst1, 4, 256);
-  k_transpose_split<<<dim3(4, 32, 4), 256, 0, stream>>>(Xp1, 1024, 256, XpS, 2048, PS1);
   k_gat_x6<<<dim3(8, 16, 4), 512, 0, stream>>>(A1, 2048, XpS, PS1, src1, dst1, P, dPp, 1024,
                                                256, 2, 512);
   k_gat_reduce<<<2048, 256, 0, stream>>>(P, 4, (size_t)2048 * 1024, dPp, (size_t)2048 * 4, bd1,
                                          X1, nullptr, 1024, 256, 2048 * 1024);
   k_score<<<512, 256, 0, stream>>>(X1, wp1, bp1, sc1, 1024);
-  k_topk_rank<<<8, 256, 2048 * 8, stream>>>(sc1, 2048, 1024, idx1, v1, nullptr);
+  k_topk_rank<<<8, 256, 2048 * 8, stream>>>(sc1, 2048, 1024, idx1, v1, inv1);
   k_gather_mat<<<dim3(4, 1024), 256, 0, stream>>>(A1, 2048, idx1, A2m, 1024);
   k_gather_scale_b16<<<dim3(1, 1024), 256, 0, stream>>>(X1, 1024, idx1, v1, X2inB);
 
   k_transpose_bf16<<<dim3(16, 16), 256, 0, stream>>>(Wb, 1024, WbT, 1024, 1024);
-  k_gemm_mfma_bt<<<dim3(8, 8), 256, 0, stream>>>(X2inB, WbT, nullptr, Xpb, 1024, 1024, 1024);
+  k_gemm_mfma_bt<<<dim3(8, 8), 256, 0, stream>>>(X2inB, WbT, nullptr, Xpb, XpT, 1024, 1024,
+                                                 1024);
   k_src_dst<<<1024, 128, 0, stream>>>(Xpb, asb, adb, srcb, dstb, 2, 512);
-  k_transpose_bf16h<<<dim3(8, 16, 2), 256, 0, stream>>>(Xpb, 1024, 512, XpT, 1024);
-  k_gat_b16<4, 1><<<dim3(2, 8, 4), 512, 0, stream>>>(A2m, 1024, XpT, srcb, dstb, P, dPp, 1024,
-                                                     512, 256);
-  k_gat_reduce<<<1024, 256, 0, stream>>>(P, 4, (size_t)1024 * 1024, dPp, (size_t)1024 * 2, bb,
+  k_gat_b16<2, 1><<<dim3(4, 8, 8), 512, 0, stream>>>(A2m, 1024, XpT, srcb, dstb, P, dPp, 1024,
+                                                     512, 128);
+  k_gat_reduce<<<1024, 256, 0, stream>>>(P, 8, (size_t)1024 * 1024, dPp, (size_t)1024 * 2, bb,
                                          nullptr, XbB, 1024, 512, 1024 * 1024);
 
   k_transpose_bf16<<<dim3(8, 16), 256, 0, stream>>>(Wu0, 512, Wu0T, 1024, 512);
-  k_gemm_mfma_bt<<<dim3(4, 8), 256, 0, stream>>>(XbB, Wu0T, nullptr, Pu0, 1024, 512, 1024);
-  k_fill0<<<1024, 256, 0, stream>>>(Xpu0, 2048 * 512);
-  k_scatter_rows<<<dim3(2, 1024), 256, 0, stream>>>(Pu0, 512, idx1, Xpu0);
+  k_gemm_mfma_bt<<<dim3(4, 8), 256, 0, stream>>>(XbB, Wu0T, nullptr, Pu0, nullptr, 1024, 512,
+                                                 1024);
+  k_unpool<<<dim3(2, 2048), 256, 0, stream>>>(Pu0, 512, inv1, Xpu0);
   k_src_dst<<<2048, 256, 0, stream>>>(Xpu0, asu0, adu0, su0, du0, 4, 128);
   k_transpose_bf16h<<<dim3(2, 32, 4), 256, 0, stream>>>(Xpu0, 512, 128, XpT, 2048);
-  k_gat_b16<4, 4><<<dim3(1, 16, 8), 512, 0, stream>>>(A1, 2048, XpT, su0, du0, P, dPp, 512,
+  k_gat_b16<2, 2><<<dim3(2, 16, 8), 512, 0, stream>>>(A1, 2048, XpT, su0, du0, P, dPp, 512,
                                                       128, 256);
   k_gat_reduce<<<1024, 256, 0, stream>>>(P, 8, (size_t)2048 * 512, dPp, (size_t)2048 * 4, bu0,
                                          nullptr, Xu0B, 512, 128, 2048 * 512);
 
   k_transpose_bf16<<<dim3(4, 8), 256, 0, stream>>>(Wu1, 256, Wu1T, 512, 256);
-  k_gemm_mfma_bt<<<dim3(2, 16), 256, 0, stream>>>(Xu0B, Wu1T, nullptr, Pu1, 2048, 256, 512);
-  k_fill0<<<1024, 256, 0, stream>>>(Xpu1, 4096 * 256);
-  k_scatter_rows<<<dim3(1, 2048), 256, 0, stream>>>(Pu1, 256, idx0, Xpu1);
+  k_gemm_mfma_bt<<<dim3(2, 16), 256, 0, stream>>>(Xu0B, Wu1T, nullptr, Pu1, nullptr, 2048, 256,
+                                                  512);
+  k_unpool<<<dim3(1, 4096), 256, 0, stream>>>(Pu1, 256, inv0, Xpu1);
   k_src_dst<<<4096, 256, 0, stream>>>(Xpu1, asu1, adu1, su1, du1, 4, 64);
   k_transpose_bf16h<<<dim3(1, 64, 4), 256, 0, stream>>>(Xpu1, 256, 64, XpT, 4096);
   k_gat_b16<2, 4><<<dim3(1, 32, 8), 512, 0, stream>>>(A0, 4096, XpT, su1, du1, P, dPp, 256,
@@ -961,8 +1027,8 @@
                                          nullptr, Xu1B, 256, 64, 4096 * 256);
   k_transpose_bb<<<dim3(4, 64), 256, 0, stream>>>(Xu1B, 256, Xu1T, 4096, 256);
 
-  k_gemm_aup<<<dim3(4, 64), 512, 0, stream>>>(Wup, Xu1T, Pz, 8192, 4096, 1024);
-  k_softmax_fuse<<<8192, 256, 0, stream>>>(Pz, 4, (size_t)8192 * 256, bup, ZB);
+  k_gemm_aup<<<dim3(8, 64), 512, 0, stream>>>(Wup, Xu1T, Pz, 8192, 4096, 512);
+  k_softmax_fuse<<<8192, 256, 0, stream>>>(Pz, 8, (size_t)8192 * 256, bup, ZB);
   k_syrk_mfma<<<dim3(64, 64), 256, 0, stream>>>(ZB, 8192, 256, Aup);
 
   k_syrk_mfma<<<dim3(32, 32), 256, 0, stream>>>(Xu1B, 4096, 256, rec1);
```

Result: slower. 1.143 ms (+19.0%).
